# Kernel optimization log

Measured on AMD Instinct MI355X. Metric: run time of the kernel, lower is better.

## Reference

```python
import jax, jax.numpy as jnp
import numpy as np

B, S, Q, D = 8, 2048, 2048, 1024  # additive path requires S == Q


def setup_inputs() -> dict:
    key = jax.random.key(0)
    ks = jax.random.split(key, 5)
    def glorot(k, shape):
        fan_in, fan_out = shape[0], shape[1]
        limit = np.sqrt(6.0 / (fan_in + fan_out)).astype(np.float32)
        return jax.random.uniform(k, shape, jnp.float32, -limit, limit)
    return {
        "source": jax.random.normal(ks[0], (B, S, D), jnp.float32),
        "query": jax.random.normal(ks[1], (B, Q, D), jnp.float32),
        "kernel": glorot(ks[2], (S, Q)),
        "wk_kernel": glorot(ks[3], (D, Q)),
        "wq_kernel": glorot(ks[4], (S, D)),
    }


def reference(source, query, kernel, wk_kernel, wq_kernel):
    # query permuted to (B, D, Q) as in call()
    q_t = jnp.transpose(query, (0, 2, 1))
    # additive similarity: tanh(Wk . Source + Wq . Query) . kernel
    f_att = (jnp.einsum("bsd,dq->bsq", source, wk_kernel)
             + jnp.einsum("sd,bdq->bsq", wq_kernel, q_t))  # (B, S, Q)
    sim = jnp.einsum("bsq,qt->bst", jnp.tanh(f_att), kernel)  # (B, S, Q)
    sm = jax.nn.softmax(sim, axis=-1)  # softmax over last axis (Keras default)
    # sm_t = permute(sm, (0,2,1)); result = batch_dot(sm_t, Source)
    return jnp.einsum("bsq,bsd->bqd", sm, source)  # (B, Q, D)
```

## Files before the change

kernel.cpp:

```cpp
#include <hip/hip_runtime.h>
#include <hip/hip_bf16.h>
#include <stdint.h>

typedef unsigned short u16;

#define B_ 8
#define S_ 2048
#define Q_ 2048
#define D_ 1024
#define T_ 2048

#define GRP 528

typedef __attribute__((ext_vector_type(8))) short short8;
typedef __attribute__((ext_vector_type(16))) float f32x16;

__device__ __forceinline__ u16 f2b(float f) {
  union { float f; uint32_t u; } x; x.f = f;
  uint32_t r = x.u + 0x7fffu + ((x.u >> 16) & 1u);
  return (u16)(r >> 16);
}
__device__ __forceinline__ float b2f(u16 h) {
  union { uint32_t u; float f; } x; x.u = ((uint32_t)h) << 16;
  return x.f;
}
__device__ __forceinline__ float tanh_fast(float x) {
  return 1.0f - 2.0f / (__expf(2.0f * x) + 1.0f);
}
__device__ __forceinline__ void async16(const void* g, void* l) {
  __builtin_amdgcn_global_load_lds(
      (const __attribute__((address_space(1))) void*)g,
      (__attribute__((address_space(3))) void*)l, 16, 0, 0);
}

__global__ void cast_f32_bf16_k(const float* __restrict__ in, u16* __restrict__ out, int n4) {
  int i = blockIdx.x * 256 + threadIdx.x;
  if (i >= n4) return;
  float4 v = ((const float4*)in)[i];
  uint32_t lo = (uint32_t)f2b(v.x) | ((uint32_t)f2b(v.y) << 16);
  uint32_t hi = (uint32_t)f2b(v.z) | ((uint32_t)f2b(v.w) << 16);
  ((uint2*)out)[i] = make_uint2(lo, hi);
}

__global__ void transpose_f32_bf16_v(const float* __restrict__ in, u16* __restrict__ out,
                                     int R, int C) {
  __shared__ u16 t[64 * 72];
  int z = blockIdx.z;
  const float* pin = in + (size_t)z * R * C;
  u16* pout = out + (size_t)z * R * C;
  int c0 = blockIdx.x * 64, r0 = blockIdx.y * 64;
  int tid = threadIdx.x;
  int rr = tid >> 4, c4 = (tid & 15) * 4;
#pragma unroll
  for (int p = 0; p < 4; ++p) {
    int r = p * 16 + rr;
    float4 v = *(const float4*)&pin[(size_t)(r0 + r) * C + c0 + c4];
    t[(c4 + 0) * 72 + r] = f2b(v.x);
    t[(c4 + 1) * 72 + r] = f2b(v.y);
    t[(c4 + 2) * 72 + r] = f2b(v.z);
    t[(c4 + 3) * 72 + r] = f2b(v.w);
  }
  __syncthreads();
  int ct = tid >> 3, r8 = (tid & 7) * 8;
#pragma unroll
  for (int p = 0; p < 2; ++p) {
    int c = p * 32 + ct;
    uint2 lo = *(const uint2*)&t[c * 72 + r8];
    uint2 hi = *(const uint2*)&t[c * 72 + r8 + 4];
    *(uint4*)&pout[(size_t)(c0 + c) * R + r0 + r8] = make_uint4(lo.x, lo.y, hi.x, hi.y);
  }
}

__global__ void src_prep_v(const float* __restrict__ in, u16* __restrict__ outc,
                           u16* __restrict__ outT) {
  __shared__ u16 t[64 * 72];
  int z = blockIdx.z;
  const float* pin = in + (size_t)z * S_ * D_;
  u16* pc = outc + (size_t)z * S_ * D_;
  u16* pt = outT + (size_t)z * S_ * D_;
  int c0 = blockIdx.x * 64, r0 = blockIdx.y * 64;
  int tid = threadIdx.x;
  int rr = tid >> 4, c4 = (tid & 15) * 4;
#pragma unroll
  for (int p = 0; p < 4; ++p) {
    int r = p * 16 + rr;
    float4 v = *(const float4*)&pin[(size_t)(r0 + r) * D_ + c0 + c4];
    u16 b0 = f2b(v.x), b1 = f2b(v.y), b2 = f2b(v.z), b3 = f2b(v.w);
    uint2 pk;
    pk.x = (uint32_t)b0 | ((uint32_t)b1 << 16);
    pk.y = (uint32_t)b2 | ((uint32_t)b3 << 16);
    *(uint2*)&pc[(size_t)(r0 + r) * D_ + c0 + c4] = pk;
    t[(c4 + 0) * 72 + r] = b0;
    t[(c4 + 1) * 72 + r] = b1;
    t[(c4 + 2) * 72 + r] = b2;
    t[(c4 + 3) * 72 + r] = b3;
  }
  __syncthreads();
  int ct = tid >> 3, r8 = (tid & 7) * 8;
#pragma unroll
  for (int p = 0; p < 2; ++p) {
    int c = p * 32 + ct;
    uint2 lo = *(const uint2*)&t[c * 72 + r8];
    uint2 hi = *(const uint2*)&t[c * 72 + r8 + 4];
    *(uint4*)&pt[(size_t)(c0 + c) * S_ + r0 + r8] = make_uint4(lo.x, lo.y, hi.x, hi.y);
  }
}

__global__ void scale_srcT_k(u16* __restrict__ srcT, const float* __restrict__ l) {
  size_t i = (size_t)blockIdx.x * 256 + threadIdx.x;
  size_t e0 = i * 8;
  int s8 = (int)(e0 & (S_ - 1));
  int bb = (int)(e0 / ((size_t)D_ * S_));
  const float* lp = l + (size_t)bb * S_ + s8;
  float4 l0 = *(const float4*)lp;
  float4 l1 = *(const float4*)(lp + 4);
  uint4 raw = *(uint4*)&srcT[e0];
  uint32_t w[4] = {raw.x, raw.y, raw.z, raw.w};
  float li[8] = {l0.x, l0.y, l0.z, l0.w, l1.x, l1.y, l1.z, l1.w};
  uint32_t o[4];
#pragma unroll
  for (int k = 0; k < 4; ++k) {
    float a = b2f((u16)(w[k] & 0xffffu)) / li[2 * k];
    float b = b2f((u16)(w[k] >> 16)) / li[2 * k + 1];
    o[k] = (uint32_t)f2b(a) | ((uint32_t)f2b(b) << 16);
  }
  *(uint4*)&srcT[e0] = make_uint4(o[0], o[1], o[2], o[3]);
}

__global__ __launch_bounds__(256, 4) void gemm_bt_k(
    const u16* __restrict__ A1, long lda1, long bsA1,
    const u16* __restrict__ B1, long ldb1, long bsB1,
    const u16* __restrict__ A2, long lda2, long bsA2,
    const u16* __restrict__ B2, long ldb2, long bsB2,
    void* __restrict__ Cv, long ldc, long bsC,
    int K, int Srows, int nTerms, int mode, float* __restrict__ lsum) {
  __shared__ __align__(16) u16 lds_all[32 * GRP];
  u16* lds_a = lds_all;
  u16* lds_b = lds_all + 16 * GRP;
  const int m0 = blockIdx.y * 128;
  const int n0 = blockIdx.x * 128;
  const int b = m0 / Srows;
  const int s0 = m0 - b * Srows;
  const int tid = threadIdx.x;
  const int wave = tid >> 6, lane = tid & 63;
  const int wm = (wave >> 1) * 64, wn = (wave & 1) * 64;
  const int l31 = lane & 31, hi = lane >> 5;
  const int srow = lane >> 3, scol = (lane & 7) * 8;

  const int rA0 = wm + l31,      rA1 = wm + 32 + l31;
  const int rB0 = wn + l31,      rB1 = wn + 32 + l31;
  const int offA0 = (rA0 >> 3) * GRP + (rA0 & 7) * 64 + hi * 8;
  const int offA1 = (rA1 >> 3) * GRP + (rA1 & 7) * 64 + hi * 8;
  const int offB0 = (rB0 >> 3) * GRP + (rB0 & 7) * 64 + hi * 8;
  const int offB1 = (rB1 >> 3) * GRP + (rB1 & 7) * 64 + hi * 8;

  f32x16 acc[2][2];
#pragma unroll
  for (int i = 0; i < 2; ++i)
#pragma unroll
    for (int j = 0; j < 2; ++j)
#pragma unroll
      for (int r = 0; r < 16; ++r) acc[i][j][r] = 0.0f;

  const u16* pA[2];
  const u16* pB[2];
  long la[2], lb[2];
  pA[0] = A1 + (size_t)bsA1 * b + (size_t)s0 * lda1;
  pB[0] = B1 + (size_t)bsB1 * b + (size_t)n0 * ldb1;
  pA[1] = (nTerms > 1) ? (A2 + (size_t)bsA2 * b + (size_t)s0 * lda2) : pA[0];
  pB[1] = (nTerms > 1) ? (B2 + (size_t)bsB2 * b + (size_t)n0 * ldb2) : pB[0];
  la[0] = lda1; la[1] = lda2;
  lb[0] = ldb1; lb[1] = ldb2;

  for (int t = 0; t < nTerms; ++t) {
    const u16* gA = pA[t];
    const u16* gB = pB[t];
    const long sA = la[t], sB = lb[t];
    for (int kt = 0; kt < K; kt += 64) {
#pragma unroll
      for (int j = 0; j < 4; ++j) {
        const int ga = j * 4 + wave;
        async16(gA + (size_t)(ga * 8 + srow) * sA + (kt + scol), &lds_a[ga * GRP]);
        async16(gB + (size_t)(ga * 8 + srow) * sB + (kt + scol), &lds_b[ga * GRP]);
      }
      __syncthreads();
#pragma unroll
      for (int kk = 0; kk < 4; ++kk) {
        short8 a0 = *(const short8*)&lds_a[offA0 + kk * 16];
        short8 a1 = *(const short8*)&lds_a[offA1 + kk * 16];
        short8 b0 = *(const short8*)&lds_b[offB0 + kk * 16];
        short8 b1 = *(const short8*)&lds_b[offB1 + kk * 16];
        acc[0][0] = __builtin_amdgcn_mfma_f32_32x32x16_bf16(a0, b0, acc[0][0], 0, 0, 0);
        acc[0][1] = __builtin_amdgcn_mfma_f32_32x32x16_bf16(a0, b1, acc[0][1], 0, 0, 0);
        acc[1][0] = __builtin_amdgcn_mfma_f32_32x32x16_bf16(a1, b0, acc[1][0], 0, 0, 0);
        acc[1][1] = __builtin_amdgcn_mfma_f32_32x32x16_bf16(a1, b1, acc[1][1], 0, 0, 0);
      }
      __syncthreads();
    }
  }

  if (mode == 3) {
#pragma unroll
    for (int mi = 0; mi < 2; ++mi)
#pragma unroll
      for (int ni = 0; ni < 2; ++ni)
#pragma unroll
        for (int r = 0; r < 16; ++r)
          acc[mi][ni][r] = __expf(acc[mi][ni][r]);
    float* lrow = lsum + (size_t)b * Srows + s0;
#pragma unroll
    for (int mi = 0; mi < 2; ++mi)
#pragma unroll
      for (int r = 0; r < 16; ++r) {
        float pv = acc[mi][0][r] + acc[mi][1][r];
        pv += __shfl_xor(pv, 1);
        pv += __shfl_xor(pv, 2);
        pv += __shfl_xor(pv, 4);
        pv += __shfl_xor(pv, 8);
        pv += __shfl_xor(pv, 16);
        const int row = wm + mi * 32 + (r & 3) + 8 * (r >> 2) + 4 * hi;
        if (l31 == 0) atomicAdd(&lrow[row], pv);
      }
#pragma unroll
    for (int mi = 0; mi < 2; ++mi)
#pragma unroll
      for (int ni = 0; ni < 2; ++ni) {
        const int col = wn + ni * 32 + l31;
#pragma unroll
        for (int g = 0; g < 4; ++g) {
          const int rowb = wm + mi * 32 + g * 8 + 4 * hi;
          u16 p0 = f2b(acc[mi][ni][g * 4 + 0]);
          u16 p1 = f2b(acc[mi][ni][g * 4 + 1]);
          u16 p2 = f2b(acc[mi][ni][g * 4 + 2]);
          u16 p3 = f2b(acc[mi][ni][g * 4 + 3]);
          uint2 pk;
          pk.x = (uint32_t)p0 | ((uint32_t)p1 << 16);
          pk.y = (uint32_t)p2 | ((uint32_t)p3 << 16);
          *(uint2*)&lds_all[col * 132 + rowb] = pk;
        }
      }
    __syncthreads();
    u16* gP = (u16*)Cv + (size_t)bsC * b + (size_t)n0 * ldc + s0;
    const int tl = tid >> 4, s8 = (tid & 15) * 8;
#pragma unroll
    for (int p = 0; p < 8; ++p) {
      const int tt = p * 16 + tl;
      uint2 lo = *(const uint2*)&lds_all[tt * 132 + s8];
      uint2 hi2 = *(const uint2*)&lds_all[tt * 132 + s8 + 4];
      *(uint4*)&gP[(size_t)tt * ldc + s8] = make_uint4(lo.x, lo.y, hi2.x, hi2.y);
    }
    return;
  }

  const size_t cbase = (size_t)bsC * b + (size_t)s0 * ldc + n0;
  if (mode == 2) {
    float* C = (float*)Cv + cbase;
#pragma unroll
    for (int mi = 0; mi < 2; ++mi)
#pragma unroll
      for (int ni = 0; ni < 2; ++ni) {
        const int col = wn + ni * 32 + l31;
#pragma unroll
        for (int r = 0; r < 16; ++r) {
          const int row = wm + mi * 32 + (r & 3) + 8 * (r >> 2) + 4 * hi;
          C[(size_t)row * ldc + col] = acc[mi][ni][r];
        }
      }
  } else {
    u16* C = (u16*)Cv + cbase;
#pragma unroll
    for (int mi = 0; mi < 2; ++mi)
#pragma unroll
      for (int ni = 0; ni < 2; ++ni) {
        const int col = wn + ni * 32 + l31;
#pragma unroll
        for (int r = 0; r < 16; ++r) {
          const int row = wm + mi * 32 + (r & 3) + 8 * (r >> 2) + 4 * hi;
          float v = acc[mi][ni][r];
          if (mode == 0) v = tanh_fast(v);
          C[(size_t)row * ldc + col] = f2b(v);
        }
      }
  }
}

extern "C" void kernel_launch(void* const* d_in, const int* in_sizes, int n_in,
                              void* d_out, int out_size, void* d_ws, size_t ws_size,
                              hipStream_t stream) {
  const float* src = (const float*)d_in[0];
  const float* qry = (const float*)d_in[1];
  const float* ker = (const float*)d_in[2];
  const float* wk  = (const float*)d_in[3];
  const float* wq  = (const float*)d_in[4];
  float* out = (float*)d_out;
  u16* ws = (u16*)d_ws;

  u16* srcb  = ws;
  u16* qryb  = srcb  + (size_t)B_ * S_ * D_;
  u16* wqb   = qryb  + (size_t)B_ * Q_ * D_;
  u16* wkT   = wqb   + (size_t)S_ * D_;
  u16* kerT  = wkT   + (size_t)D_ * Q_;
  u16* srcT  = kerT  + (size_t)Q_ * T_;
  u16* tanhT = srcT  + (size_t)B_ * D_ * S_;
  u16* PT    = tanhT + (size_t)B_ * S_ * Q_;
  float* l   = (float*)(PT + (size_t)B_ * T_ * S_);

  dim3 tb(256);

  cast_f32_bf16_k<<<(B_ * Q_ * D_) / 1024, 256, 0, stream>>>(qry, qryb, (B_ * Q_ * D_) / 4);
  cast_f32_bf16_k<<<(S_ * D_) / 1024, 256, 0, stream>>>(wq, wqb, (S_ * D_) / 4);
  transpose_f32_bf16_v<<<dim3(Q_ / 64, D_ / 64, 1), tb, 0, stream>>>(wk, wkT, D_, Q_);
  transpose_f32_bf16_v<<<dim3(T_ / 64, Q_ / 64, 1), tb, 0, stream>>>(ker, kerT, Q_, T_);
  src_prep_v<<<dim3(D_ / 64, S_ / 64, B_), tb, 0, stream>>>(src, srcb, srcT);
  hipMemsetAsync(l, 0, (size_t)B_ * S_ * sizeof(float), stream);

  gemm_bt_k<<<dim3(Q_ / 128, (B_ * S_) / 128), 256, 0, stream>>>(
      srcb, D_, (long)S_ * D_,
      wkT, D_, 0,
      wqb, D_, 0,
      qryb, D_, (long)Q_ * D_,
      tanhT, Q_, (long)S_ * Q_,
      D_, S_, 2, 0, nullptr);

  gemm_bt_k<<<dim3(T_ / 128, (B_ * S_) / 128), 256, 0, stream>>>(
      tanhT, Q_, (long)S_ * Q_,
      kerT, Q_, 0,
      nullptr, 0, 0, nullptr, 0, 0,
      PT, S_, (long)T_ * S_,
      Q_, S_, 1, 3, l);

  scale_srcT_k<<<(B_ * D_ * S_) / (256 * 8), 256, 0, stream>>>(srcT, l);

  gemm_bt_k<<<dim3(D_ / 128, (B_ * T_) / 128), 256, 0, stream>>>(
      PT, S_, (long)T_ * S_,
      srcT, S_, (long)D_ * S_,
      nullptr, 0, 0, nullptr, 0, 0,
      out, D_, (long)T_ * D_,
      S_, T_, 1, 2, nullptr);
}
```

Measured before the change: 618.4 us.

## Replace GEMM with 256x256 tile, 8-wave, double-buffered pipelined MFMA kernel

```diff
diff --git a/kernel.cpp b/kernel.cpp
--- a/kernel.cpp
+++ b/kernel.cpp
@@ -9,8 +9,6 @@
 #define Q_ 2048
 #define D_ 1024
 #define T_ 2048
-
-#define GRP 528
 
 typedef __attribute__((ext_vector_type(8))) short short8;
 typedef __attribute__((ext_vector_type(16))) float f32x16;
@@ -127,89 +125,157 @@
   *(uint4*)&srcT[e0] = make_uint4(o[0], o[1], o[2], o[3]);
 }
 
-__global__ __launch_bounds__(256, 4) void gemm_bt_k(
+__global__ __launch_bounds__(512, 2) void gemm256_k(
     const u16* __restrict__ A1, long lda1, long bsA1,
     const u16* __restrict__ B1, long ldb1, long bsB1,
     const u16* __restrict__ A2, long lda2, long bsA2,
     const u16* __restrict__ B2, long ldb2, long bsB2,
     void* __restrict__ Cv, long ldc, long bsC,
     int K, int Srows, int nTerms, int mode, float* __restrict__ lsum) {
-  __shared__ __align__(16) u16 lds_all[32 * GRP];
-  u16* lds_a = lds_all;
-  u16* lds_b = lds_all + 16 * GRP;
-  const int m0 = blockIdx.y * 128;
-  const int n0 = blockIdx.x * 128;
+  __shared__ __align__(16) u16 lds[65536];
+
+  const int tid = threadIdx.x;
+  const int w = tid >> 6, lane = tid & 63;
+  const int wr = w >> 2, wc = w & 3;
+  const int l31 = lane & 31, hi = lane >> 5;
+
+  const int gx = gridDim.x;
+  const int nwg = gx * (int)gridDim.y;
+  int lid = blockIdx.y * gx + blockIdx.x;
+  if ((nwg & 7) == 0) lid = (lid & 7) * (nwg >> 3) + (lid >> 3);
+  const int bn = lid % gx, bm = lid / gx;
+  const int n0 = bn * 256, m0 = bm * 256;
   const int b = m0 / Srows;
   const int s0 = m0 - b * Srows;
-  const int tid = threadIdx.x;
-  const int wave = tid >> 6, lane = tid & 63;
-  const int wm = (wave >> 1) * 64, wn = (wave & 1) * 64;
-  const int l31 = lane & 31, hi = lane >> 5;
-  const int srow = lane >> 3, scol = (lane & 7) * 8;
-
-  const int rA0 = wm + l31,      rA1 = wm + 32 + l31;
-  const int rB0 = wn + l31,      rB1 = wn + 32 + l31;
-  const int offA0 = (rA0 >> 3) * GRP + (rA0 & 7) * 64 + hi * 8;
-  const int offA1 = (rA1 >> 3) * GRP + (rA1 & 7) * 64 + hi * 8;
-  const int offB0 = (rB0 >> 3) * GRP + (rB0 & 7) * 64 + hi * 8;
-  const int offB1 = (rB1 >> 3) * GRP + (rB1 & 7) * 64 + hi * 8;
-
-  f32x16 acc[2][2];
-#pragma unroll
-  for (int i = 0; i < 2; ++i)
-#pragma unroll
-    for (int j = 0; j < 2; ++j)
-#pragma unroll
-      for (int r = 0; r < 16; ++r) acc[i][j][r] = 0.0f;
-
-  const u16* pA[2];
-  const u16* pB[2];
-  long la[2], lb[2];
-  pA[0] = A1 + (size_t)bsA1 * b + (size_t)s0 * lda1;
-  pB[0] = B1 + (size_t)bsB1 * b + (size_t)n0 * ldb1;
-  pA[1] = (nTerms > 1) ? (A2 + (size_t)bsA2 * b + (size_t)s0 * lda2) : pA[0];
-  pB[1] = (nTerms > 1) ? (B2 + (size_t)bsB2 * b + (size_t)n0 * ldb2) : pB[0];
-  la[0] = lda1; la[1] = lda2;
-  lb[0] = ldb1; lb[1] = ldb2;
-
-  for (int t = 0; t < nTerms; ++t) {
-    const u16* gA = pA[t];
-    const u16* gB = pB[t];
-    const long sA = la[t], sB = lb[t];
-    for (int kt = 0; kt < K; kt += 64) {
-#pragma unroll
-      for (int j = 0; j < 4; ++j) {
-        const int ga = j * 4 + wave;
-        async16(gA + (size_t)(ga * 8 + srow) * sA + (kt + scol), &lds_a[ga * GRP]);
-        async16(gB + (size_t)(ga * 8 + srow) * sB + (kt + scol), &lds_b[ga * GRP]);
-      }
-      __syncthreads();
-#pragma unroll
-      for (int kk = 0; kk < 4; ++kk) {
-        short8 a0 = *(const short8*)&lds_a[offA0 + kk * 16];
-        short8 a1 = *(const short8*)&lds_a[offA1 + kk * 16];
-        short8 b0 = *(const short8*)&lds_b[offB0 + kk * 16];
-        short8 b1 = *(const short8*)&lds_b[offB1 + kk * 16];
-        acc[0][0] = __builtin_amdgcn_mfma_f32_32x32x16_bf16(a0, b0, acc[0][0], 0, 0, 0);
-        acc[0][1] = __builtin_amdgcn_mfma_f32_32x32x16_bf16(a0, b1, acc[0][1], 0, 0, 0);
-        acc[1][0] = __builtin_amdgcn_mfma_f32_32x32x16_bf16(a1, b0, acc[1][0], 0, 0, 0);
-        acc[1][1] = __builtin_amdgcn_mfma_f32_32x32x16_bf16(a1, b1, acc[1][1], 0, 0, 0);
-      }
-      __syncthreads();
+
+  const int ktiles = K >> 6;
+  const int ktlog = __ffs(ktiles) - 1;
+  const int ktmask = ktiles - 1;
+  const int NT = nTerms * ktiles;
+
+  const u16* gA1 = A1 + (size_t)bsA1 * b + (size_t)s0 * lda1;
+  const u16* gB1 = B1 + (size_t)bsB1 * b + (size_t)n0 * ldb1;
+  const u16* gA2 = (nTerms > 1) ? (A2 + (size_t)bsA2 * b + (size_t)s0 * lda2) : gA1;
+  const u16* gB2 = (nTerms > 1) ? (B2 + (size_t)bsB2 * b + (size_t)n0 * ldb2) : gB1;
+
+  const int lrow = lane >> 3, lslot = lane & 7;
+  const int gsl = (lslot ^ lrow) << 3;
+
+  auto STG = [&](int tile, int isB, int half) {
+    if (tile >= NT) return;
+    const int term = tile >> ktlog;
+    const int kt = (tile & ktmask) << 6;
+    const u16* g = isB ? (term ? gB2 : gB1) : (term ? gA2 : gA1);
+    const long ld = isB ? (term ? ldb2 : ldb1) : (term ? lda2 : lda1);
+    u16* lb = lds + ((tile & 1) << 15) + (isB << 14);
+#pragma unroll
+    for (int is = 0; is < 2; ++is) {
+      const int rh0 = is * 64 + w * 8;
+      const int r0 = isB ? (half * 32 + (rh0 & 31) + ((rh0 >> 5) << 6))
+                         : (half * 64 + (rh0 & 63) + ((rh0 >> 6) << 7));
+      async16(g + (size_t)(r0 + lrow) * ld + kt + gsl, lb + r0 * 64);
     }
+  };
+
+  f32x16 acc[4][2];
+#pragma unroll
+  for (int x = 0; x < 4; ++x)
+#pragma unroll
+    for (int y = 0; y < 2; ++y)
+#pragma unroll
+      for (int r = 0; r < 16; ++r) acc[x][y][r] = 0.0f;
+
+  u16* bufXA = lds;
+  u16* bufXB = lds + 16384;
+  u16* bufYA = lds + 32768;
+  u16* bufYB = lds + 49152;
+
+  const int aR = (wr * 128 + l31) * 64;
+  const int bR = (wc * 64 + l31) * 64;
+  int soff[4];
+#pragma unroll
+  for (int kk = 0; kk < 4; ++kk)
+    soff[kk] = ((((kk << 1) | hi) ^ (l31 & 7)) << 3);
+
+  short8 av[2][4], bv[4];
+
+#define RD_A(bufA, mh)                                                        \
+  _Pragma("unroll") for (int m = 0; m < 2; ++m)                               \
+  _Pragma("unroll") for (int kk = 0; kk < 4; ++kk)                            \
+      av[m][kk] = *(const short8*)&(bufA)[aR + ((mh)*2 + m) * 2048 + soff[kk]];
+#define RD_B(bufB, nh)                                                        \
+  _Pragma("unroll") for (int kk = 0; kk < 4; ++kk)                            \
+      bv[kk] = *(const short8*)&(bufB)[bR + (nh)*2048 + soff[kk]];
+#define BAR                              \
+  __builtin_amdgcn_sched_barrier(0);     \
+  __builtin_amdgcn_s_barrier();          \
+  __builtin_amdgcn_sched_barrier(0)
+#define MFMA8(mh, nh)                                                         \
+  __builtin_amdgcn_s_setprio(1);                                              \
+  _Pragma("unroll") for (int kk = 0; kk < 4; ++kk)                            \
+  _Pragma("unroll") for (int m = 0; m < 2; ++m)                               \
+      acc[(mh)*2 + m][nh] = __builtin_amdgcn_mfma_f32_32x32x16_bf16(          \
+          av[m][kk], bv[kk], acc[(mh)*2 + m][nh], 0, 0, 0);                   \
+  __builtin_amdgcn_s_setprio(0)
+#define VMC4                                         \
+  asm volatile("s_waitcnt vmcnt(4)" ::: "memory");   \
+  __builtin_amdgcn_sched_barrier(0)
+
+  STG(0, 0, 0); STG(0, 1, 1); STG(0, 0, 1); STG(0, 1, 0);
+  STG(1, 0, 0); STG(1, 1, 1);
+  VMC4;
+  BAR;
+
+  const int niter = NT >> 1;
+  for (int i = 0; i < niter; ++i) {
+    const int u = 2 * i;
+    RD_A(bufXA, 0); RD_B(bufXB, 0);
+    STG(u + 1, 0, 1);
+    BAR; MFMA8(0, 0); BAR;
+
+    RD_B(bufXB, 1);
+    STG(u + 1, 1, 0);
+    BAR; MFMA8(0, 1); BAR;
+
+    RD_A(bufXA, 1);
+    STG(u + 2, 0, 0);
+    BAR; MFMA8(1, 1); BAR;
+
+    RD_B(bufXB, 0);
+    STG(u + 2, 1, 1);
+    BAR; MFMA8(1, 0);
+    VMC4;
+    BAR;
+
+    RD_A(bufYA, 0); RD_B(bufYB, 0);
+    STG(u + 2, 0, 1);
+    BAR; MFMA8(0, 0); BAR;
+
+    RD_B(bufYB, 1);
+    STG(u + 2, 1, 0);
+    BAR; MFMA8(0, 1); BAR;
+
+    RD_A(bufYA, 1);
+    STG(u + 3, 0, 0);
+    BAR; MFMA8(1, 1); BAR;
+
+    RD_B(bufYB, 0);
+    STG(u + 3, 1, 1);
+    BAR; MFMA8(1, 0);
+    VMC4;
+    BAR;
   }
 
   if (mode == 3) {
 #pragma unroll
-    for (int mi = 0; mi < 2; ++mi)
+    for (int mi = 0; mi < 4; ++mi)
 #pragma unroll
       for (int ni = 0; ni < 2; ++ni)
 #pragma unroll
-        for (int r = 0; r < 16; ++r)
-          acc[mi][ni][r] = __expf(acc[mi][ni][r]);
-    float* lrow = lsum + (size_t)b * Srows + s0;
-#pragma unroll
-    for (int mi = 0; mi < 2; ++mi)
+        for (int r = 0; r < 16; ++r) acc[mi][ni][r] = __expf(acc[mi][ni][r]);
+    float* lrowp = lsum + (size_t)b * Srows + s0;
+#pragma unroll
+    for (int mi = 0; mi < 4; ++mi)
 #pragma unroll
       for (int r = 0; r < 16; ++r) {
         float pv = acc[mi][0][r] + acc[mi][1][r];
@@ -218,64 +284,74 @@
         pv += __shfl_xor(pv, 4);
         pv += __shfl_xor(pv, 8);
         pv += __shfl_xor(pv, 16);
-        const int row = wm + mi * 32 + (r & 3) + 8 * (r >> 2) + 4 * hi;
-        if (l31 == 0) atomicAdd(&lrow[row], pv);
-      }
-#pragma unroll
-    for (int mi = 0; mi < 2; ++mi)
-#pragma unroll
-      for (int ni = 0; ni < 2; ++ni) {
-        const int col = wn + ni * 32 + l31;
-#pragma unroll
-        for (int g = 0; g < 4; ++g) {
-          const int rowb = wm + mi * 32 + g * 8 + 4 * hi;
-          u16 p0 = f2b(acc[mi][ni][g * 4 + 0]);
-          u16 p1 = f2b(acc[mi][ni][g * 4 + 1]);
-          u16 p2 = f2b(acc[mi][ni][g * 4 + 2]);
-          u16 p3 = f2b(acc[mi][ni][g * 4 + 3]);
-          uint2 pk;
-          pk.x = (uint32_t)p0 | ((uint32_t)p1 << 16);
-          pk.y = (uint32_t)p2 | ((uint32_t)p3 << 16);
-          *(uint2*)&lds_all[col * 132 + rowb] = pk;
+        if (l31 == 0) {
+          const int row = wr * 128 + mi * 32 + (r & 3) + 8 * (r >> 2) + 4 * hi;
+          atomicAdd(&lrowp[row], pv);
         }
       }
+    u16* gP = (u16*)Cv + (size_t)bsC * b + (size_t)n0 * ldc + s0;
     __syncthreads();
-    u16* gP = (u16*)Cv + (size_t)bsC * b + (size_t)n0 * ldc + s0;
-    const int tl = tid >> 4, s8 = (tid & 15) * 8;
-#pragma unroll
-    for (int p = 0; p < 8; ++p) {
-      const int tt = p * 16 + tl;
-      uint2 lo = *(const uint2*)&lds_all[tt * 132 + s8];
-      uint2 hi2 = *(const uint2*)&lds_all[tt * 132 + s8 + 4];
-      *(uint4*)&gP[(size_t)tt * ldc + s8] = make_uint4(lo.x, lo.y, hi2.x, hi2.y);
+#pragma unroll
+    for (int p = 0; p < 2; ++p) {
+      if ((wc >> 1) == p) {
+#pragma unroll
+        for (int mi = 0; mi < 4; ++mi)
+#pragma unroll
+          for (int ni = 0; ni < 2; ++ni) {
+            const int tc = (wc & 1) * 64 + ni * 32 + l31;
+#pragma unroll
+            for (int g2 = 0; g2 < 4; ++g2) {
+              const int sr = wr * 128 + mi * 32 + g2 * 8 + hi * 4;
+              u16 p0 = f2b(acc[mi][ni][g2 * 4 + 0]);
+              u16 p1 = f2b(acc[mi][ni][g2 * 4 + 1]);
+              u16 p2 = f2b(acc[mi][ni][g2 * 4 + 2]);
+              u16 p3 = f2b(acc[mi][ni][g2 * 4 + 3]);
+              uint2 pk;
+              pk.x = (uint32_t)p0 | ((uint32_t)p1 << 16);
+              pk.y = (uint32_t)p2 | ((uint32_t)p3 << 16);
+              *(uint2*)&lds[tc * 268 + sr] = pk;
+            }
+          }
+      }
+      __syncthreads();
+#pragma unroll
+      for (int j = 0; j < 8; ++j) {
+        const int idx = j * 512 + tid;
+        const int tt = idx >> 5, s8 = (idx & 31) * 8;
+        uint2 lo = *(const uint2*)&lds[tt * 268 + s8];
+        uint2 h2 = *(const uint2*)&lds[tt * 268 + s8 + 4];
+        *(uint4*)&gP[(size_t)(p * 128 + tt) * ldc + s8] =
+            make_uint4(lo.x, lo.y, h2.x, h2.y);
+      }
+      __syncthreads();
     }
     return;
   }
 
-  const size_t cbase = (size_t)bsC * b + (size_t)s0 * ldc + n0;
+  const size_t cb = (size_t)bsC * b + (size_t)s0 * ldc + n0;
   if (mode == 2) {
-    float* C = (float*)Cv + cbase;
-#pragma unroll
-    for (int mi = 0; mi < 2; ++mi)
+    float* C = (float*)Cv + cb;
+#pragma unroll
+    for (int mi = 0; mi < 4; ++mi)
 #pragma unroll
       for (int ni = 0; ni < 2; ++ni) {
-        const int col = wn + ni * 32 + l31;
+        const int col = wc * 64 + ni * 32 + l31;
 #pragma unroll
         for (int r = 0; r < 16; ++r) {
-          const int row = wm + mi * 32 + (r & 3) + 8 * (r >> 2) + 4 * hi;
+          const int row = wr * 128 + mi * 32 + (r & 3) + 8 * (r >> 2) + 4 * hi;
           C[(size_t)row * ldc + col] = acc[mi][ni][r];
         }
       }
   } else {
-    u16* C = (u16*)Cv + cbase;
-#pragma unroll
-    for (int mi = 0; mi < 2; ++mi)
+    u16* C = (u16*)Cv + cb;
+#pragma unroll
+    for (int mi = 0; mi < 4; ++mi)
 #pragma unroll
       for (int ni = 0; ni < 2; ++ni) {
-        const int col = wn + ni * 32 + l31;
+        const int col = wc * 64 + ni * 32 + l31;
 #pragma unroll
         for (int r = 0; r < 16; ++r) {
-          const int row = wm + mi * 32 + (r & 3) + 8 * (r >> 2) + 4 * hi;
+          const int row = wr * 128 + mi * 32 + (r & 3) + 8 * (r >> 2) + 4 * hi;
           float v = acc[mi][ni][r];
           if (mode == 0) v = tanh_fast(v);
           C[(size_t)row * ldc + col] = f2b(v);
@@ -283,6 +359,12 @@
       }
   }
 }
+
+#undef RD_A
+#undef RD_B
+#undef BAR
+#undef MFMA8
+#undef VMC4
 
 extern "C" void kernel_launch(void* const* d_in, const int* in_sizes, int n_in,
                               void* d_out, int out_size, void* d_ws, size_t ws_size,
@@ -314,7 +396,7 @@
   src_prep_v<<<dim3(D_ / 64, S_ / 64, B_), tb, 0, stream>>>(src, srcb, srcT);
   hipMemsetAsync(l, 0, (size_t)B_ * S_ * sizeof(float), stream);
 
-  gemm_bt_k<<<dim3(Q_ / 128, (B_ * S_) / 128), 256, 0, stream>>>(
+  gemm256_k<<<dim3(Q_ / 256, (B_ * S_) / 256), 512, 0, stream>>>(
       srcb, D_, (long)S_ * D_,
       wkT, D_, 0,
       wqb, D_, 0,
@@ -322,7 +404,7 @@
       tanhT, Q_, (long)S_ * Q_,
       D_, S_, 2, 0, nullptr);
 
-  gemm_bt_k<<<dim3(T_ / 128, (B_ * S_) / 128), 256, 0, stream>>>(
+  gemm256_k<<<dim3(T_ / 256, (B_ * S_) / 256), 512, 0, stream>>>(
       tanhT, Q_, (long)S_ * Q_,
       kerT, Q_, 0,
       nullptr, 0, 0, nullptr, 0, 0,
@@ -331,7 +413,7 @@
 
   scale_srcT_k<<<(B_ * D_ * S_) / (256 * 8), 256, 0, stream>>>(srcT, l);
 
-  gemm_bt_k<<<dim3(D_ / 128, (B_ * T_) / 128), 256, 0, stream>>>(
+  gemm256_k<<<dim3(D_ / 256, (B_ * T_) / 256), 512, 0, stream>>>(
       PT, S_, (long)T_ * S_,
       srcT, S_, (long)D_ * S_,
       nullptr, 0, 0, nullptr, 0, 0,
```

Result: no change. 629.9 us (+1.9%).
